# Optimization experiments

Measured on AMD Instinct MI355X. Metric: run time of the kernel, lower is better.

## Reference

```python
import jax, jax.numpy as jnp
import numpy as np

LOG100 = float(np.log(100.0))
EPS = 1e-12  # F.normalize eps


def _l2norm(x):
    # torch.nn.functional.normalize(x, dim=-1): x / max(||x||_2, eps)
    n = jnp.sqrt(jnp.sum(x * x, axis=-1, keepdims=True))
    return x / jnp.maximum(n, EPS)


def setup_inputs() -> dict:
    key = jax.random.key(0)
    k1, k2, k3, k4, k5 = jax.random.split(key, 5)
    B_, nH, N, d = 256, 8, 256, 64
    q = jax.random.normal(k1, (B_, nH, N, d), dtype=jnp.float32)
    k = jax.random.normal(k2, (B_, nH, N, d), dtype=jnp.float32)
    v = jax.random.normal(k3, (B_, nH, N, d), dtype=jnp.float32)
    logit_scale = jax.random.normal(k4, (nH, 1, 1), dtype=jnp.float32)
    bias = jax.random.normal(k5, (nH, N, N), dtype=jnp.float32)
    return {"q": q, "k": k, "v": v, "logit_scale": logit_scale, "bias": bias}


def reference(q, k, v, logit_scale, bias):
    B_, nH, N, d = q.shape
    # cosine-similarity attention (euclidean_dist=False branch)
    scores = jnp.einsum("bhnd,bhmd->bhnm", _l2norm(q), _l2norm(k))
    # attn_transform: Swin-v2-style clamped learned logit scale + rel-pos bias
    scale = jnp.exp(jnp.minimum(logit_scale, LOG100))  # (nH,1,1)
    scores = scores * scale[None] + bias[None]
    attn = jax.nn.softmax(scores, axis=-1)
    # attn_drop with p=0 is identity
    x = jnp.einsum("bhnm,bhmd->bhnd", attn, v)
    # reshape=True branch: x.transpose(1,2).reshape(B_, -1, H*head_dim) with H==N
    x = jnp.transpose(x, (0, 2, 1, 3)).reshape(B_, -1, N * d)  # (B_, nH, N*d)
    return x
```

## Files before the change

### kernel.cpp

```cpp
#include <hip/hip_runtime.h>

#define LOG100 4.605170185988091f
#define LOG2E  1.4426950408889634f

typedef _Float16 half8 __attribute__((ext_vector_type(8)));
typedef float f32x16 __attribute__((ext_vector_type(16)));

__global__ __launch_bounds__(256) void bias_transpose(const float* __restrict__ bias,
                                                      float* __restrict__ biasT) {
  __shared__ float tile[32][33];
  const int head = blockIdx.z;
  const int m0 = blockIdx.x * 32;
  const int n0 = blockIdx.y * 32;
  const float* src = bias + head * 65536;
  float* dst = biasT + head * 65536;
  const int tx = threadIdx.x, ty = threadIdx.y;
#pragma unroll
  for (int i = ty; i < 32; i += 8) tile[i][tx] = src[(n0 + i) * 256 + m0 + tx];
  __syncthreads();
#pragma unroll
  for (int i = ty; i < 32; i += 8) dst[(m0 + i) * 256 + n0 + tx] = tile[tx][i] * LOG2E;
}

template <bool USE_BT>
__global__ __launch_bounds__(512, 4) void attn_kernel(
    const float* __restrict__ q, const float* __restrict__ k, const float* __restrict__ v,
    const float* __restrict__ logit_scale, const float* __restrict__ bias,
    const float* __restrict__ biasT, float* __restrict__ out) {
  __shared__ __align__(16) char smem[65536];
  _Float16* Kn = (_Float16*)smem;
  _Float16* Vt = (_Float16*)(smem + 32768);

  const int tid = threadIdx.x;
  const int wave = tid >> 6;
  const int lane = tid & 63;
  const int l31 = lane & 31;
  const int hi = lane >> 5;
  const int head = blockIdx.x;
  const int b = blockIdx.y;

  const long base = ((long)(b * 8 + head)) * (256 * 64);
  const float* qp = q + base;
  const float* kp = k + base;
  const float* vp = v + base;

  const float scale2 = __expf(fminf(logit_scale[head], LOG100)) * LOG2E;

  const int qrow = wave * 32 + l31;
  half8 qfrag[4];
  {
    float qf[4][8];
    float ssq = 0.f;
#pragma unroll
    for (int dk = 0; dk < 4; ++dk) {
      const float4 x0 = *(const float4*)(qp + qrow * 64 + dk * 16 + hi * 8);
      const float4 x1 = *(const float4*)(qp + qrow * 64 + dk * 16 + hi * 8 + 4);
      qf[dk][0] = x0.x; qf[dk][1] = x0.y; qf[dk][2] = x0.z; qf[dk][3] = x0.w;
      qf[dk][4] = x1.x; qf[dk][5] = x1.y; qf[dk][6] = x1.z; qf[dk][7] = x1.w;
      ssq += x0.x * x0.x + x0.y * x0.y + x0.z * x0.z + x0.w * x0.w;
      ssq += x1.x * x1.x + x1.y * x1.y + x1.z * x1.z + x1.w * x1.w;
    }
    ssq += __shfl_xor(ssq, 32);
    const float qinv = rsqrtf(fmaxf(ssq, 1e-24f));
#pragma unroll
    for (int dk = 0; dk < 4; ++dk)
#pragma unroll
      for (int j = 0; j < 8; ++j) qfrag[dk][j] = (_Float16)(qf[dk][j] * qinv);
  }

  {
    const int row_in = tid >> 4;
    const int seg = tid & 15;
#pragma unroll
    for (int it = 0; it < 8; ++it) {
      const int row = it * 32 + row_in;
      const float4 a = *(const float4*)(kp + row * 64 + seg * 4);
      float ss = a.x * a.x + a.y * a.y + a.z * a.z + a.w * a.w;
      ss += __shfl_xor(ss, 1);
      ss += __shfl_xor(ss, 2);
      ss += __shfl_xor(ss, 4);
      ss += __shfl_xor(ss, 8);
      const float inv = rsqrtf(fmaxf(ss, 1e-24f));
      union { _Float16 hh[4]; uint2 u; } pk4;
      pk4.hh[0] = (_Float16)(a.x * inv);
      pk4.hh[1] = (_Float16)(a.y * inv);
      pk4.hh[2] = (_Float16)(a.z * inv);
      pk4.hh[3] = (_Float16)(a.w * inv);
      char* wp = (char*)Kn + row * 128 + ((seg * 8) ^ ((row & 15) << 3));
      *(uint2*)wp = pk4.u;
    }
  }

  {
    const int r = lane >> 4;
    const int sx = lane & 15;
#pragma unroll
    for (int it = 0; it < 8; ++it) {
      const int kv0 = (wave * 8 + it) * 4;
      float4 a = *(const float4*)(vp + (kv0 + r) * 64 + sx * 4);
      float e1 = (r & 1) ? a.x : a.y;
      float g1 = __shfl_xor(e1, 16);
      float e2 = (r & 1) ? a.z : a.w;
      float g2 = __shfl_xor(e2, 16);
      if (r & 1) { a.x = g1; a.z = g2; } else { a.y = g1; a.w = g2; }
      float e3 = (r & 2) ? a.x : a.z;
      float g3 = __shfl_xor(e3, 32);
      float e4 = (r & 2) ? a.y : a.w;
      float g4 = __shfl_xor(e4, 32);
      if (r & 2) { a.x = g3; a.y = g4; } else { a.z = g3; a.w = g4; }
      const int d = 4 * sx + r;
      union { _Float16 hh[4]; uint2 u; } pk4;
      pk4.hh[0] = (_Float16)a.x;
      pk4.hh[1] = (_Float16)a.y;
      pk4.hh[2] = (_Float16)a.z;
      pk4.hh[3] = (_Float16)a.w;
      char* wp = (char*)Vt + d * 512 + ((kv0 * 2) ^ ((d & 31) << 4));
      *(uint2*)wp = pk4.u;
    }
  }

  __syncthreads();

  f32x16 o0 = {};
  f32x16 o1 = {};
  float m = -1.0e30f, lsum = 0.f;

  const float* bT;
  if (USE_BT)
    bT = biasT + head * 65536 + (4 * hi) * 256 + qrow;
  else
    bT = bias + head * 65536 + qrow * 256 + 4 * hi;

  for (int c = 0; c < 8; ++c) {
    float bv[16];
#pragma unroll
    for (int reg = 0; reg < 16; ++reg) {
      const int kvr = (reg & 3) + 8 * (reg >> 2);
      bv[reg] = USE_BT ? bT[(c * 32 + kvr) * 256] : bT[c * 32 + kvr] * LOG2E;
    }

    const int krow = c * 32 + l31;
    const char* kbase = (const char*)Kn + krow * 128;
    const int kmsk = (krow & 15) << 3;
    f32x16 s = {};
    __builtin_amdgcn_s_setprio(1);
#pragma unroll
    for (int dk = 0; dk < 4; ++dk) {
      union { uint2 u[2]; half8 hh; } kf;
      kf.u[0] = *(const uint2*)(kbase + ((dk * 32 + hi * 16) ^ kmsk));
      kf.u[1] = *(const uint2*)(kbase + ((dk * 32 + hi * 16 + 8) ^ kmsk));
      s = __builtin_amdgcn_mfma_f32_32x32x16_f16(kf.hh, qfrag[dk], s, 0, 0, 0);
    }
    __builtin_amdgcn_s_setprio(0);

#pragma unroll
    for (int reg = 0; reg < 16; ++reg) s[reg] = fmaf(s[reg], scale2, bv[reg]);

    float m8[8];
#pragma unroll
    for (int i = 0; i < 8; ++i) m8[i] = fmaxf(s[2 * i], s[2 * i + 1]);
    float m4[4];
#pragma unroll
    for (int i = 0; i < 4; ++i) m4[i] = fmaxf(m8[2 * i], m8[2 * i + 1]);
    float mx = fmaxf(fmaxf(m4[0], m4[1]), fmaxf(m4[2], m4[3]));
    mx = fmaxf(mx, __shfl_xor(mx, 32));

    if (__any(mx > m + 8.0f)) {
      const float mnew = fmaxf(m, mx);
      const float corr = exp2f(m - mnew);
      lsum *= corr;
#pragma unroll
      for (int i = 0; i < 16; ++i) { o0[i] *= corr; o1[i] *= corr; }
      m = mnew;
    }

#pragma unroll
    for (int reg = 0; reg < 16; ++reg) s[reg] = exp2f(s[reg] - m);
    float a8[8];
#pragma unroll
    for (int i = 0; i < 8; ++i) a8[i] = s[2 * i] + s[2 * i + 1];
    float a4[4];
#pragma unroll
    for (int i = 0; i < 4; ++i) a4[i] = a8[2 * i] + a8[2 * i + 1];
    float psum = (a4[0] + a4[1]) + (a4[2] + a4[3]);
    psum += __shfl_xor(psum, 32);
    lsum += psum;

    unsigned pk[8];
#pragma unroll
    for (int i = 0; i < 8; ++i)
      pk[i] = __builtin_bit_cast(unsigned, __builtin_amdgcn_cvt_pkrtz(s[2 * i], s[2 * i + 1]));
    const unsigned ra = __shfl_xor(hi ? pk[0] : pk[2], 32);
    const unsigned rb = __shfl_xor(hi ? pk[1] : pk[3], 32);
    const unsigned rc = __shfl_xor(hi ? pk[4] : pk[6], 32);
    const unsigned rd = __shfl_xor(hi ? pk[5] : pk[7], 32);
    union { unsigned u[4]; half8 hh; } f0, f1;
    f0.u[0] = hi ? ra : pk[0];
    f0.u[1] = hi ? rb : pk[1];
    f0.u[2] = hi ? pk[2] : ra;
    f0.u[3] = hi ? pk[3] : rb;
    f1.u[0] = hi ? rc : pk[4];
    f1.u[1] = hi ? rd : pk[5];
    f1.u[2] = hi ? pk[6] : rc;
    f1.u[3] = hi ? pk[7] : rd;

    {
      const int d = l31;
      const char* vbase = (const char*)Vt + d * 512;
      const int msk = (d & 31) << 4;
      const half8 vf0 = *(const half8*)(vbase + ((c * 64 + hi * 16) ^ msk));
      const half8 vf1 = *(const half8*)(vbase + ((c * 64 + 32 + hi * 16) ^ msk));
      __builtin_amdgcn_s_setprio(1);
      o0 = __builtin_amdgcn_mfma_f32_32x32x16_f16(vf0, f0.hh, o0, 0, 0, 0);
      o0 = __builtin_amdgcn_mfma_f32_32x32x16_f16(vf1, f1.hh, o0, 0, 0, 0);
      __builtin_amdgcn_s_setprio(0);
    }
    {
      const int d = 32 + l31;
      const char* vbase = (const char*)Vt + d * 512;
      const int msk = (d & 31) << 4;
      const half8 vf0 = *(const half8*)(vbase + ((c * 64 + hi * 16) ^ msk));
      const half8 vf1 = *(const half8*)(vbase + ((c * 64 + 32 + hi * 16) ^ msk));
      __builtin_amdgcn_s_setprio(1);
      o1 = __builtin_amdgcn_mfma_f32_32x32x16_f16(vf0, f0.hh, o1, 0, 0, 0);
      o1 = __builtin_amdgcn_mfma_f32_32x32x16_f16(vf1, f1.hh, o1, 0, 0, 0);
      __builtin_amdgcn_s_setprio(0);
    }
  }

  __syncthreads();

  char* ob = (char*)smem + wave * 4096;
  const float invl = 1.0f / lsum;
#pragma unroll
  for (int r = 0; r < 16; r += 2) {
    const int d0 = (r & 3) + 8 * (r >> 2) + 4 * hi;
    const unsigned w0 =
        __builtin_bit_cast(unsigned, __builtin_amdgcn_cvt_pkrtz(o0[r] * invl, o0[r + 1] * invl));
    *(unsigned*)(ob + l31 * 128 + ((d0 * 2) ^ ((l31 & 15) << 3))) = w0;
    const unsigned w1 =
        __builtin_bit_cast(unsigned, __builtin_amdgcn_cvt_pkrtz(o1[r] * invl, o1[r + 1] * invl));
    *(unsigned*)(ob + l31 * 128 + (((d0 + 32) * 2) ^ ((l31 & 15) << 3))) = w1;
  }
  __asm__ __volatile__("s_waitcnt lgkmcnt(0)" ::: "memory");
  __builtin_amdgcn_sched_barrier(0);
  const int sx = lane & 15;
  const int rr = lane >> 4;
#pragma unroll
  for (int kq = 0; kq < 8; ++kq) {
    const int qq = kq * 4 + rr;
    union { uint2 u; _Float16 hh[4]; } rd4;
    rd4.u = *(const uint2*)(ob + qq * 128 + ((sx * 8) ^ ((qq & 15) << 3)));
    float4 val;
    val.x = (float)rd4.hh[0];
    val.y = (float)rd4.hh[1];
    val.z = (float)rd4.hh[2];
    val.w = (float)rd4.hh[3];
    *(float4*)(out + (((long)(b * 256 + wave * 32 + qq) * 8 + head) * 64 + 4 * sx)) = val;
  }
}

extern "C" void kernel_launch(void* const* d_in, const int* in_sizes, int n_in,
                              void* d_out, int out_size, void* d_ws, size_t ws_size,
                              hipStream_t stream) {
  (void)in_sizes; (void)n_in; (void)out_size;
  const float* q = (const float*)d_in[0];
  const float* k = (const float*)d_in[1];
  const float* v = (const float*)d_in[2];
  const float* ls = (const float*)d_in[3];
  const float* bias = (const float*)d_in[4];
  float* out = (float*)d_out;
  const size_t btBytes = (size_t)8 * 256 * 256 * 4;
  if (ws_size >= btBytes) {
    float* biasT = (float*)d_ws;
    bias_transpose<<<dim3(8, 8, 8), dim3(32, 8), 0, stream>>>(bias, biasT);
    attn_kernel<true><<<dim3(8, 256), dim3(512), 0, stream>>>(q, k, v, ls, bias, biasT, out);
  } else {
    attn_kernel<false><<<dim3(8, 256), dim3(512), 0, stream>>>(q, k, v, ls, bias, nullptr, out);
  }
}
```

Measured before the change: 147.5 us.

## Pack bias to fp16 pairs and stage K/V in two halves to halve LDS

The bias pre-pass now stores the transposed, log2e-scaled bias as packed fp16 pairs, so the attention kernel reads half as many bias bytes per score tile. The K/V staging is split into two 128-row halves processed sequentially with an extra barrier, cutting shared memory from 64KB to 32KB per block, which should allow more blocks per CU. In exchange, bias precision drops to fp16 and each block serializes two load/compute phases with an added sync.

```diff
diff --git a/kernel.cpp b/kernel.cpp
--- a/kernel.cpp
+++ b/kernel.cpp
@@ -6,30 +6,35 @@
 typedef _Float16 half8 __attribute__((ext_vector_type(8)));
 typedef float f32x16 __attribute__((ext_vector_type(16)));
 
-__global__ __launch_bounds__(256) void bias_transpose(const float* __restrict__ bias,
-                                                      float* __restrict__ biasT) {
+__global__ __launch_bounds__(256) void bias_pack(const float* __restrict__ bias,
+                                                 unsigned* __restrict__ biasP) {
   __shared__ float tile[32][33];
   const int head = blockIdx.z;
   const int m0 = blockIdx.x * 32;
   const int n0 = blockIdx.y * 32;
   const float* src = bias + head * 65536;
-  float* dst = biasT + head * 65536;
+  unsigned* dst = biasP + head * 32768;
   const int tx = threadIdx.x, ty = threadIdx.y;
 #pragma unroll
   for (int i = ty; i < 32; i += 8) tile[i][tx] = src[(n0 + i) * 256 + m0 + tx];
   __syncthreads();
 #pragma unroll
-  for (int i = ty; i < 32; i += 8) dst[(m0 + i) * 256 + n0 + tx] = tile[tx][i] * LOG2E;
+  for (int j = ty; j < 16; j += 8) {
+    const float lo = tile[tx][2 * j] * LOG2E;
+    const float hi = tile[tx][2 * j + 1] * LOG2E;
+    dst[(m0 / 2 + j) * 256 + n0 + tx] =
+        __builtin_bit_cast(unsigned, __builtin_amdgcn_cvt_pkrtz(lo, hi));
+  }
 }
 
 template <bool USE_BT>
 __global__ __launch_bounds__(512, 4) void attn_kernel(
     const float* __restrict__ q, const float* __restrict__ k, const float* __restrict__ v,
     const float* __restrict__ logit_scale, const float* __restrict__ bias,
-    const float* __restrict__ biasT, float* __restrict__ out) {
-  __shared__ __align__(16) char smem[65536];
+    const unsigned* __restrict__ biasP, float* __restrict__ out) {
+  __shared__ __align__(16) char smem[32768];
   _Float16* Kn = (_Float16*)smem;
-  _Float16* Vt = (_Float16*)(smem + 32768);
+  _Float16* Vt = (_Float16*)(smem + 16384);
 
   const int tid = threadIdx.x;
   const int wave = tid >> 6;
@@ -68,163 +73,183 @@
       for (int j = 0; j < 8; ++j) qfrag[dk][j] = (_Float16)(qf[dk][j] * qinv);
   }
 
-  {
-    const int row_in = tid >> 4;
-    const int seg = tid & 15;
-#pragma unroll
-    for (int it = 0; it < 8; ++it) {
-      const int row = it * 32 + row_in;
-      const float4 a = *(const float4*)(kp + row * 64 + seg * 4);
-      float ss = a.x * a.x + a.y * a.y + a.z * a.z + a.w * a.w;
-      ss += __shfl_xor(ss, 1);
-      ss += __shfl_xor(ss, 2);
-      ss += __shfl_xor(ss, 4);
-      ss += __shfl_xor(ss, 8);
-      const float inv = rsqrtf(fmaxf(ss, 1e-24f));
-      union { _Float16 hh[4]; uint2 u; } pk4;
-      pk4.hh[0] = (_Float16)(a.x * inv);
-      pk4.hh[1] = (_Float16)(a.y * inv);
-      pk4.hh[2] = (_Float16)(a.z * inv);
-      pk4.hh[3] = (_Float16)(a.w * inv);
-      char* wp = (char*)Kn + row * 128 + ((seg * 8) ^ ((row & 15) << 3));
-      *(uint2*)wp = pk4.u;
-    }
-  }
-
-  {
-    const int r = lane >> 4;
-    const int sx = lane & 15;
-#pragma unroll
-    for (int it = 0; it < 8; ++it) {
-      const int kv0 = (wave * 8 + it) * 4;
-      float4 a = *(const float4*)(vp + (kv0 + r) * 64 + sx * 4);
-      float e1 = (r & 1) ? a.x : a.y;
-      float g1 = __shfl_xor(e1, 16);
-      float e2 = (r & 1) ? a.z : a.w;
-      float g2 = __shfl_xor(e2, 16);
-      if (r & 1) { a.x = g1; a.z = g2; } else { a.y = g1; a.w = g2; }
-      float e3 = (r & 2) ? a.x : a.z;
-      float g3 = __shfl_xor(e3, 32);
-      float e4 = (r & 2) ? a.y : a.w;
-      float g4 = __shfl_xor(e4, 32);
-      if (r & 2) { a.x = g3; a.y = g4; } else { a.z = g3; a.w = g4; }
-      const int d = 4 * sx + r;
-      union { _Float16 hh[4]; uint2 u; } pk4;
-      pk4.hh[0] = (_Float16)a.x;
-      pk4.hh[1] = (_Float16)a.y;
-      pk4.hh[2] = (_Float16)a.z;
-      pk4.hh[3] = (_Float16)a.w;
-      char* wp = (char*)Vt + d * 512 + ((kv0 * 2) ^ ((d & 31) << 4));
-      *(uint2*)wp = pk4.u;
-    }
-  }
-
-  __syncthreads();
-
   f32x16 o0 = {};
   f32x16 o1 = {};
   float m = -1.0e30f, lsum = 0.f;
 
-  const float* bT;
-  if (USE_BT)
-    bT = biasT + head * 65536 + (4 * hi) * 256 + qrow;
-  else
-    bT = bias + head * 65536 + qrow * 256 + 4 * hi;
-
-  for (int c = 0; c < 8; ++c) {
-    float bv[16];
-#pragma unroll
-    for (int reg = 0; reg < 16; ++reg) {
-      const int kvr = (reg & 3) + 8 * (reg >> 2);
-      bv[reg] = USE_BT ? bT[(c * 32 + kvr) * 256] : bT[c * 32 + kvr] * LOG2E;
+  const unsigned* bP = USE_BT ? (biasP + head * 32768 + qrow) : nullptr;
+  const float* bF = USE_BT ? nullptr : (bias + head * 65536 + qrow * 256 + 4 * hi);
+
+  for (int h = 0; h < 2; ++h) {
+    if (h) __syncthreads();
+
+    {
+      const int row_in = tid >> 4;
+      const int seg = tid & 15;
+#pragma unroll
+      for (int it = 0; it < 4; ++it) {
+        const int r = it * 32 + row_in;
+        const float4 a = *(const float4*)(kp + (h * 128 + r) * 64 + seg * 4);
+        float ss = a.x * a.x + a.y * a.y + a.z * a.z + a.w * a.w;
+        ss += __shfl_xor(ss, 1);
+        ss += __shfl_xor(ss, 2);
+        ss += __shfl_xor(ss, 4);
+        ss += __shfl_xor(ss, 8);
+        const float inv = rsqrtf(fmaxf(ss, 1e-24f));
+        union { _Float16 hh[4]; uint2 u; } pk4;
+        pk4.hh[0] = (_Float16)(a.x * inv);
+        pk4.hh[1] = (_Float16)(a.y * inv);
+        pk4.hh[2] = (_Float16)(a.z * inv);
+        pk4.hh[3] = (_Float16)(a.w * inv);
+        char* wp = (char*)Kn + r * 128 + ((seg * 8) ^ ((r & 15) << 3));
+        *(uint2*)wp = pk4.u;
+      }
     }
 
-    const int krow = c * 32 + l31;
-    const char* kbase = (const char*)Kn + krow * 128;
-    const int kmsk = (krow & 15) << 3;
-    f32x16 s = {};
-    __builtin_amdgcn_s_setprio(1);
-#pragma unroll
-    for (int dk = 0; dk < 4; ++dk) {
-      union { uint2 u[2]; half8 hh; } kf;
-      kf.u[0] = *(const uint2*)(kbase + ((dk * 32 + hi * 16) ^ kmsk));
-      kf.u[1] = *(const uint2*)(kbase + ((dk * 32 + hi * 16 + 8) ^ kmsk));
-      s = __builtin_amdgcn_mfma_f32_32x32x16_f16(kf.hh, qfrag[dk], s, 0, 0, 0);
+    {
+      const int r = lane >> 4;
+      const int sx = lane & 15;
+#pragma unroll
+      for (int it = 0; it < 4; ++it) {
+        const int kv0 = (wave * 4 + it) * 4;
+        float4 a = *(const float4*)(vp + (h * 128 + kv0 + r) * 64 + sx * 4);
+        float e1 = (r & 1) ? a.x : a.y;
+        float g1 = __shfl_xor(e1, 16);
+        float e2 = (r & 1) ? a.z : a.w;
+        float g2 = __shfl_xor(e2, 16);
+        if (r & 1) { a.x = g1; a.z = g2; } else { a.y = g1; a.w = g2; }
+        float e3 = (r & 2) ? a.x : a.z;
+        float g3 = __shfl_xor(e3, 32);
+        float e4 = (r & 2) ? a.y : a.w;
+        float g4 = __shfl_xor(e4, 32);
+        if (r & 2) { a.x = g3; a.y = g4; } else { a.z = g3; a.w = g4; }
+        const int d = 4 * sx + r;
+        union { _Float16 hh[4]; uint2 u; } pk4;
+        pk4.hh[0] = (_Float16)a.x;
+        pk4.hh[1] = (_Float16)a.y;
+        pk4.hh[2] = (_Float16)a.z;
+        pk4.hh[3] = (_Float16)a.w;
+        char* wp = (char*)Vt + d * 256 + ((kv0 * 2) ^ ((d & 15) << 4));
+        *(uint2*)wp = pk4.u;
+      }
     }
-    __builtin_amdgcn_s_setprio(0);
-
-#pragma unroll
-    for (int reg = 0; reg < 16; ++reg) s[reg] = fmaf(s[reg], scale2, bv[reg]);
-
-    float m8[8];
-#pragma unroll
-    for (int i = 0; i < 8; ++i) m8[i] = fmaxf(s[2 * i], s[2 * i + 1]);
-    float m4[4];
-#pragma unroll
-    for (int i = 0; i < 4; ++i) m4[i] = fmaxf(m8[2 * i], m8[2 * i + 1]);
-    float mx = fmaxf(fmaxf(m4[0], m4[1]), fmaxf(m4[2], m4[3]));
-    mx = fmaxf(mx, __shfl_xor(mx, 32));
-
-    if (__any(mx > m + 8.0f)) {
-      const float mnew = fmaxf(m, mx);
-      const float corr = exp2f(m - mnew);
-      lsum *= corr;
-#pragma unroll
-      for (int i = 0; i < 16; ++i) { o0[i] *= corr; o1[i] *= corr; }
-      m = mnew;
-    }
-
-#pragma unroll
-    for (int reg = 0; reg < 16; ++reg) s[reg] = exp2f(s[reg] - m);
-    float a8[8];
-#pragma unroll
-    for (int i = 0; i < 8; ++i) a8[i] = s[2 * i] + s[2 * i + 1];
-    float a4[4];
-#pragma unroll
-    for (int i = 0; i < 4; ++i) a4[i] = a8[2 * i] + a8[2 * i + 1];
-    float psum = (a4[0] + a4[1]) + (a4[2] + a4[3]);
-    psum += __shfl_xor(psum, 32);
-    lsum += psum;
-
-    unsigned pk[8];
-#pragma unroll
-    for (int i = 0; i < 8; ++i)
-      pk[i] = __builtin_bit_cast(unsigned, __builtin_amdgcn_cvt_pkrtz(s[2 * i], s[2 * i + 1]));
-    const unsigned ra = __shfl_xor(hi ? pk[0] : pk[2], 32);
-    const unsigned rb = __shfl_xor(hi ? pk[1] : pk[3], 32);
-    const unsigned rc = __shfl_xor(hi ? pk[4] : pk[6], 32);
-    const unsigned rd = __shfl_xor(hi ? pk[5] : pk[7], 32);
-    union { unsigned u[4]; half8 hh; } f0, f1;
-    f0.u[0] = hi ? ra : pk[0];
-    f0.u[1] = hi ? rb : pk[1];
-    f0.u[2] = hi ? pk[2] : ra;
-    f0.u[3] = hi ? pk[3] : rb;
-    f1.u[0] = hi ? rc : pk[4];
-    f1.u[1] = hi ? rd : pk[5];
-    f1.u[2] = hi ? pk[6] : rc;
-    f1.u[3] = hi ? pk[7] : rd;
-
-    {
-      const int d = l31;
-      const char* vbase = (const char*)Vt + d * 512;
-      const int msk = (d & 31) << 4;
-      const half8 vf0 = *(const half8*)(vbase + ((c * 64 + hi * 16) ^ msk));
-      const half8 vf1 = *(const half8*)(vbase + ((c * 64 + 32 + hi * 16) ^ msk));
+
+    __syncthreads();
+
+    for (int c = 0; c < 4; ++c) {
+      unsigned bw[8];
+      float bvf[16];
+      if (USE_BT) {
+#pragma unroll
+        for (int i = 0; i < 8; ++i) {
+          const int kp_off = (i & 1) + 4 * (i >> 1) + 2 * hi;
+          bw[i] = bP[(h * 64 + c * 16 + kp_off) * 256];
+        }
+      } else {
+        const int kvg = h * 128 + c * 32;
+#pragma unroll
+        for (int reg = 0; reg < 16; ++reg) {
+          const int kvr = (reg & 3) + 8 * (reg >> 2);
+          bvf[reg] = bF[kvg + kvr] * LOG2E;
+        }
+      }
+
+      const int krow = c * 32 + l31;
+      const char* kbase = (const char*)Kn + krow * 128;
+      const int kmsk = (krow & 15) << 3;
+      f32x16 s = {};
       __builtin_amdgcn_s_setprio(1);
-      o0 = __builtin_amdgcn_mfma_f32_32x32x16_f16(vf0, f0.hh, o0, 0, 0, 0);
-      o0 = __builtin_amdgcn_mfma_f32_32x32x16_f16(vf1, f1.hh, o0, 0, 0, 0);
+#pragma unroll
+      for (int dk = 0; dk < 4; ++dk) {
+        union { uint2 u[2]; half8 hh; } kf;
+        kf.u[0] = *(const uint2*)(kbase + ((dk * 32 + hi * 16) ^ kmsk));
+        kf.u[1] = *(const uint2*)(kbase + ((dk * 32 + hi * 16 + 8) ^ kmsk));
+        s = __builtin_amdgcn_mfma_f32_32x32x16_f16(kf.hh, qfrag[dk], s, 0, 0, 0);
+      }
       __builtin_amdgcn_s_setprio(0);
-    }
-    {
-      const int d = 32 + l31;
-      const char* vbase = (const char*)Vt + d * 512;
-      const int msk = (d & 31) << 4;
-      const half8 vf0 = *(const half8*)(vbase + ((c * 64 + hi * 16) ^ msk));
-      const half8 vf1 = *(const half8*)(vbase + ((c * 64 + 32 + hi * 16) ^ msk));
-      __builtin_amdgcn_s_setprio(1);
-      o1 = __builtin_amdgcn_mfma_f32_32x32x16_f16(vf0, f0.hh, o1, 0, 0, 0);
-      o1 = __builtin_amdgcn_mfma_f32_32x32x16_f16(vf1, f1.hh, o1, 0, 0, 0);
-      __builtin_amdgcn_s_setprio(0);
+
+      if (USE_BT) {
+#pragma unroll
+        for (int i = 0; i < 8; ++i) {
+          const _Float16* hp = (const _Float16*)&bw[i];
+          s[2 * i] = fmaf(s[2 * i], scale2, (float)hp[0]);
+          s[2 * i + 1] = fmaf(s[2 * i + 1], scale2, (float)hp[1]);
+        }
+      } else {
+#pragma unroll
+        for (int reg = 0; reg < 16; ++reg) s[reg] = fmaf(s[reg], scale2, bvf[reg]);
+      }
+
+      float m8[8];
+#pragma unroll
+      for (int i = 0; i < 8; ++i) m8[i] = fmaxf(s[2 * i], s[2 * i + 1]);
+      float m4[4];
+#pragma unroll
+      for (int i = 0; i < 4; ++i) m4[i] = fmaxf(m8[2 * i], m8[2 * i + 1]);
+      float mx = fmaxf(fmaxf(m4[0], m4[1]), fmaxf(m4[2], m4[3]));
+      mx = fmaxf(mx, __shfl_xor(mx, 32));
+
+      if (__any(mx > m + 8.0f)) {
+        const float mnew = fmaxf(m, mx);
+        const float corr = exp2f(m - mnew);
+        lsum *= corr;
+#pragma unroll
+        for (int i = 0; i < 16; ++i) { o0[i] *= corr; o1[i] *= corr; }
+        m = mnew;
+      }
+
+#pragma unroll
+      for (int reg = 0; reg < 16; ++reg) s[reg] = exp2f(s[reg] - m);
+      float a8[8];
+#pragma unroll
+      for (int i = 0; i < 8; ++i) a8[i] = s[2 * i] + s[2 * i + 1];
+      float a4[4];
+#pragma unroll
+      for (int i = 0; i < 4; ++i) a4[i] = a8[2 * i] + a8[2 * i + 1];
+      float psum = (a4[0] + a4[1]) + (a4[2] + a4[3]);
+      psum += __shfl_xor(psum, 32);
+      lsum += psum;
+
+      unsigned pk[8];
+#pragma unroll
+      for (int i = 0; i < 8; ++i)
+        pk[i] = __builtin_bit_cast(unsigned, __builtin_amdgcn_cvt_pkrtz(s[2 * i], s[2 * i + 1]));
+      const unsigned ra = __shfl_xor(hi ? pk[0] : pk[2], 32);
+      const unsigned rb = __shfl_xor(hi ? pk[1] : pk[3], 32);
+      const unsigned rc = __shfl_xor(hi ? pk[4] : pk[6], 32);
+      const unsigned rd = __shfl_xor(hi ? pk[5] : pk[7], 32);
+      union { unsigned u[4]; half8 hh; } f0, f1;
+      f0.u[0] = hi ? ra : pk[0];
+      f0.u[1] = hi ? rb : pk[1];
+      f0.u[2] = hi ? pk[2] : ra;
+      f0.u[3] = hi ? pk[3] : rb;
+      f1.u[0] = hi ? rc : pk[4];
+      f1.u[1] = hi ? rd : pk[5];
+      f1.u[2] = hi ? pk[6] : rc;
+      f1.u[3] = hi ? pk[7] : rd;
+
+      {
+        const int d = l31;
+        const char* vbase = (const char*)Vt + d * 256;
+        const int msk = (d & 15) << 4;
+        const half8 vf0 = *(const half8*)(vbase + ((c * 64 + hi * 16) ^ msk));
+        const half8 vf1 = *(const half8*)(vbase + ((c * 64 + 32 + hi * 16) ^ msk));
+        __builtin_amdgcn_s_setprio(1);
+        o0 = __builtin_amdgcn_mfma_f32_32x32x16_f16(vf0, f0.hh, o0, 0, 0, 0);
+        o0 = __builtin_amdgcn_mfma_f32_32x32x16_f16(vf1, f1.hh, o0, 0, 0, 0);
+        __builtin_amdgcn_s_setprio(0);
+      }
+      {
+        const int d = 32 + l31;
+        const char* vbase = (const char*)Vt + d * 256;
+        const int msk = (d & 15) << 4;
+        const half8 vf0 = *(const half8*)(vbase + ((c * 64 + hi * 16) ^ msk));
+        const half8 vf1 = *(const half8*)(vbase + ((c * 64 + 32 + hi * 16) ^ msk));
+        __builtin_amdgcn_s_setprio(1);
+        o1 = __builtin_amdgcn_mfma_f32_32x32x16_f16(vf0, f0.hh, o1, 0, 0, 0);
+        o1 = __builtin_amdgcn_mfma_f32_32x32x16_f16(vf1, f1.hh, o1, 0, 0, 0);
+        __builtin_amdgcn_s_setprio(0);
+      }
     }
   }
 
@@ -270,11 +295,11 @@
   const float* ls = (const float*)d_in[3];
   const float* bias = (const float*)d_in[4];
   float* out = (float*)d_out;
-  const size_t btBytes = (size_t)8 * 256 * 256 * 4;
-  if (ws_size >= btBytes) {
-    float* biasT = (float*)d_ws;
-    bias_transpose<<<dim3(8, 8, 8), dim3(32, 8), 0, stream>>>(bias, biasT);
-    attn_kernel<true><<<dim3(8, 256), dim3(512), 0, stream>>>(q, k, v, ls, bias, biasT, out);
+  const size_t bpBytes = (size_t)8 * 128 * 256 * 4;
+  if (ws_size >= bpBytes) {
+    unsigned* biasP = (unsigned*)d_ws;
+    bias_pack<<<dim3(8, 8, 8), dim3(32, 8), 0, stream>>>(bias, biasP);
+    attn_kernel<true><<<dim3(8, 256), dim3(512), 0, stream>>>(q, k, v, ls, bias, biasP, out);
   } else {
     attn_kernel<false><<<dim3(8, 256), dim3(512), 0, stream>>>(q, k, v, ls, bias, nullptr, out);
   }
```

Measured after the change: 176.7 us. +19.8%, slower.
